# Performance work log

Hardware: AMD Instinct MI355X
Metric: run time of the kernel (lower is better)

## Reference

```python
import jax, jax.numpy as jnp
import numpy as np

BZ, C, H, W, M = 8, 64, 64, 64, 2048  # N = H*W = 4096 scene-graph nodes


def setup_inputs() -> dict:
    key = jax.random.key(0)
    k1, k2 = jax.random.split(key)
    sg_node_feats = jax.random.normal(k1, (BZ, C, H, W), dtype=jnp.float32)
    # weighted adjacency from SG nodes (N) to KG nodes (M)
    sg_kg_adj = jax.random.uniform(k2, (BZ, H * W, M), dtype=jnp.float32)
    return {"sg_node_feats": sg_node_feats, "sg_kg_adj": sg_kg_adj}


def reference(sg_node_feats, sg_kg_adj):
    bz, channels, height, width = sg_node_feats.shape
    x = sg_node_feats.reshape(bz, channels, height * width)  # (bz, C, N)
    degrees = sg_kg_adj.sum(axis=1)                          # (bz, M)
    norm = jnp.maximum(degrees, 1.0)                         # (bz, M)
    # broadcast-multiply + sum over N == batched GEMM (bz,C,N) x (bz,N,M)
    out = jnp.einsum('bcn,bnm->bcm', x, sg_kg_adj) / norm[:, None, :]
    return out.transpose(0, 2, 1)                            # (bz, M, C)
```

## Files before the change

kernel.cpp:

```cpp
#include <hip/hip_runtime.h>


typedef short bf16x8 __attribute__((ext_vector_type(8)));
typedef float f32x4 __attribute__((ext_vector_type(4)));

#define BZc 8
#define Cc 64
#define Nc 4096
#define Mc 2048
#define BMc 64
#define BKc 64
#define KITERS (Nc / BKc)
#define SDW 36

__device__ __forceinline__ unsigned int pkbf(float a, float b) {
  unsigned int ua = __float_as_uint(a) + 0x8000u;
  unsigned int ub = __float_as_uint(b) + 0x8000u;
  return (ua >> 16) | (ub & 0xffff0000u);
}

__global__ __launch_bounds__(512) void sgkg_kernel(
    const float* __restrict__ x,
    const float* __restrict__ adj,
    float* __restrict__ out)
{
  __shared__ unsigned int adjT[BMc * SDW];
  __shared__ float degs[BMc];

  const int t = threadIdx.x;
  const int l = t & 63;
  const int w = t >> 6;

  const int bz     = blockIdx.x >> 5;
  const int m_base = (blockIdx.x & 31) * BMc;

  const int mg  = ((w & 1) << 3) | (l & 7);
  const int p   = ((w >> 1) << 3) | (l >> 3);
  const int sm0 = mg << 2;

  const float* aptr =
      adj + (size_t)bz * Nc * Mc + (size_t)(2 * p) * Mc + (m_base + sm0);
  const int wb = SDW * sm0 + ((((p >> 2) ^ (mg & 7))) << 2) + (p & 3);

  const int m_off = (w & 1) << 5;
  const int c_b   = (w >> 1) << 4;
  const int l15   = l & 15;
  const int l4    = l >> 4;

  const float* xb =
      x + ((size_t)bz * Cc + (c_b + l15)) * Nc + (l4 << 3);

  int aaddr[2][2];
#pragma unroll
  for (int tm = 0; tm < 2; ++tm) {
    const int m  = m_off + tm * 16 + l15;
    const int pi = (m >> 2) & 7;
    aaddr[tm][0] = SDW * m + (((l4) ^ pi) << 2);
    aaddr[tm][1] = SDW * m + (((4 + l4) ^ pi) << 2);
  }

  if (t < BMc) degs[t] = 0.0f;

  f32x4 acc0 = {0.f, 0.f, 0.f, 0.f};
  f32x4 acc1 = {0.f, 0.f, 0.f, 0.f};
  float dacc0 = 0.f, dacc1 = 0.f, dacc2 = 0.f, dacc3 = 0.f;

  float4 r0 = *(const float4*)aptr;
  float4 r1 = *(const float4*)(aptr + Mc);

  for (int it = 0; it < KITERS; ++it) {
    __syncthreads();

    adjT[wb          ] = pkbf(r0.x, r1.x);
    adjT[wb +     SDW] = pkbf(r0.y, r1.y);
    adjT[wb + 2 * SDW] = pkbf(r0.z, r1.z);
    adjT[wb + 3 * SDW] = pkbf(r0.w, r1.w);

    dacc0 += r0.x + r1.x;
    dacc1 += r0.y + r1.y;
    dacc2 += r0.z + r1.z;
    dacc3 += r0.w + r1.w;

    const float* anext = (it + 1 < KITERS) ? (aptr + (size_t)BKc * Mc) : aptr;
    float4 s0 = *(const float4*)anext;
    float4 s1 = *(const float4*)(anext + Mc);

    const float* xit = xb + it * BKc;
    float4 blo0 = *(const float4*)(xit);
    float4 bhi0 = *(const float4*)(xit + 4);
    float4 blo1 = *(const float4*)(xit + 32);
    float4 bhi1 = *(const float4*)(xit + 36);
    union { uint4 u; bf16x8 v; } B0, B1;
    B0.u = make_uint4(pkbf(blo0.x, blo0.y), pkbf(blo0.z, blo0.w),
                      pkbf(bhi0.x, bhi0.y), pkbf(bhi0.z, bhi0.w));
    B1.u = make_uint4(pkbf(blo1.x, blo1.y), pkbf(blo1.z, blo1.w),
                      pkbf(bhi1.x, bhi1.y), pkbf(bhi1.z, bhi1.w));

    __syncthreads();

    bf16x8 a00 = *(const bf16x8*)(adjT + aaddr[0][0]);
    bf16x8 a10 = *(const bf16x8*)(adjT + aaddr[1][0]);
    acc0 = __builtin_amdgcn_mfma_f32_16x16x32_bf16(a00, B0.v, acc0, 0, 0, 0);
    acc1 = __builtin_amdgcn_mfma_f32_16x16x32_bf16(a10, B0.v, acc1, 0, 0, 0);
    bf16x8 a01 = *(const bf16x8*)(adjT + aaddr[0][1]);
    bf16x8 a11 = *(const bf16x8*)(adjT + aaddr[1][1]);
    acc0 = __builtin_amdgcn_mfma_f32_16x16x32_bf16(a01, B1.v, acc0, 0, 0, 0);
    acc1 = __builtin_amdgcn_mfma_f32_16x16x32_bf16(a11, B1.v, acc1, 0, 0, 0);

    aptr = anext;
    r0 = s0;
    r1 = s1;
  }

  __syncthreads();
  atomicAdd(&degs[sm0 + 0], dacc0);
  atomicAdd(&degs[sm0 + 1], dacc1);
  atomicAdd(&degs[sm0 + 2], dacc2);
  atomicAdd(&degs[sm0 + 3], dacc3);
  __syncthreads();

#pragma unroll
  for (int tm = 0; tm < 2; ++tm) {
    const f32x4 acc = tm ? acc1 : acc0;
#pragma unroll
    for (int r = 0; r < 4; ++r) {
      const int ml    = m_off + tm * 16 + (l4 << 2) + r;
      const float nrm = fmaxf(degs[ml], 1.0f);
      const float v   = acc[r] / nrm;
      const size_t o  = ((size_t)(bz * Mc + m_base + ml)) * Cc + (c_b + l15);
      out[o] = v;
    }
  }
}

extern "C" void kernel_launch(void* const* d_in, const int* in_sizes, int n_in,
                              void* d_out, int out_size, void* d_ws, size_t ws_size,
                              hipStream_t stream) {
  const float* x   = (const float*)d_in[0];
  const float* adj = (const float*)d_in[1];
  float* out       = (float*)d_out;
  (void)in_sizes; (void)n_in; (void)out_size; (void)d_ws; (void)ws_size;

  sgkg_kernel<<<dim3(BZc * (Mc / BMc)), dim3(512), 0, stream>>>(x, adj, out);
}
```

Baseline: 378.1 us.

## Split N across blocks, pre-convert x to bf16, double-buffer LDS, add reduce kernel

Adds a pre-pass kernel that converts x to bf16 in workspace so the main loop loads packed bf16 directly instead of converting fp32 every iteration. The main GEMM now uses a split-K over N (two halves) with smaller 32-row M tiles and 256-thread blocks, giving four times as many blocks. The LDS tile is double-buffered, which removes one barrier per iteration. Partial sums and degrees go to workspace and a final kernel adds them and normalizes, at the cost of two extra launches and extra global traffic for the partials.

```diff
diff --git a/kernel.cpp b/kernel.cpp
--- a/kernel.cpp
+++ b/kernel.cpp
@@ -8,10 +8,19 @@
 #define Cc 64
 #define Nc 4096
 #define Mc 2048
-#define BMc 64
+#define BMc 32
 #define BKc 64
-#define KITERS (Nc / BKc)
+#define NSPLIT 2
+#define NSc (Nc / NSPLIT)
+#define KITERS (NSc / BKc)
 #define SDW 36
+#define TILE_DW (BMc * SDW)
+
+#define WS_X_BYTES   (BZc * Cc * Nc * 2)
+#define WS_P_FLOATS  (BZc * Mc * Cc)
+#define WS_P_OFF     (WS_X_BYTES / 4)
+#define WS_D_OFF     (WS_P_OFF + NSPLIT * WS_P_FLOATS)
+#define WS_D_FLOATS  (BZc * Mc)
 
 __device__ __forceinline__ unsigned int pkbf(float a, float b) {
   unsigned int ua = __float_as_uint(a) + 0x8000u;
@@ -19,43 +28,56 @@
   return (ua >> 16) | (ub & 0xffff0000u);
 }
 
-__global__ __launch_bounds__(512) void sgkg_kernel(
-    const float* __restrict__ x,
+__global__ __launch_bounds__(256) void xcvt_kernel(const float* __restrict__ x,
+                                                   unsigned int* __restrict__ xb) {
+  const int i = (blockIdx.x * 256 + threadIdx.x) * 8;
+  float4 a = *(const float4*)(x + i);
+  float4 b = *(const float4*)(x + i + 4);
+  uint4 o = make_uint4(pkbf(a.x, a.y), pkbf(a.z, a.w),
+                       pkbf(b.x, b.y), pkbf(b.z, b.w));
+  *(uint4*)(xb + (i >> 1)) = o;
+}
+
+__global__ __launch_bounds__(256) void sgkg_main(
+    const unsigned int* __restrict__ xbw,
     const float* __restrict__ adj,
-    float* __restrict__ out)
+    float* __restrict__ P,
+    float* __restrict__ D)
 {
-  __shared__ unsigned int adjT[BMc * SDW];
+  __shared__ unsigned int adjT[2][TILE_DW];
   __shared__ float degs[BMc];
 
   const int t = threadIdx.x;
   const int l = t & 63;
   const int w = t >> 6;
 
-  const int bz     = blockIdx.x >> 5;
-  const int m_base = (blockIdx.x & 31) * BMc;
+  const int bz     = blockIdx.x >> 7;
+  const int mb     = (blockIdx.x >> 1) & 63;
+  const int ns     = blockIdx.x & 1;
+  const int m_base = mb * BMc;
+  const int n_base = ns * NSc;
 
-  const int mg  = ((w & 1) << 3) | (l & 7);
-  const int p   = ((w >> 1) << 3) | (l >> 3);
+  const int mg  = l & 7;
+  const int p   = (w << 3) | (l >> 3);
   const int sm0 = mg << 2;
 
   const float* aptr =
-      adj + (size_t)bz * Nc * Mc + (size_t)(2 * p) * Mc + (m_base + sm0);
-  const int wb = SDW * sm0 + ((((p >> 2) ^ (mg & 7))) << 2) + (p & 3);
+      adj + (size_t)bz * Nc * Mc + (size_t)(n_base + 2 * p) * Mc + (m_base + sm0);
+  const int wb = SDW * sm0 + (((p >> 2) ^ mg) << 2) + (p & 3);
 
-  const int m_off = (w & 1) << 5;
-  const int c_b   = (w >> 1) << 4;
-  const int l15   = l & 15;
-  const int l4    = l >> 4;
+  const int c_b = w << 4;
+  const int l15 = l & 15;
+  const int l4  = l >> 4;
 
-  const float* xb =
-      x + ((size_t)bz * Cc + (c_b + l15)) * Nc + (l4 << 3);
+  const uint4* xq = (const uint4*)xbw +
+      (size_t)(bz * Cc + c_b + l15) * (Nc / 8) + (n_base >> 3) + l4;
 
   int aaddr[2][2];
 #pragma unroll
   for (int tm = 0; tm < 2; ++tm) {
-    const int m  = m_off + tm * 16 + l15;
+    const int m  = tm * 16 + l15;
     const int pi = (m >> 2) & 7;
-    aaddr[tm][0] = SDW * m + (((l4) ^ pi) << 2);
+    aaddr[tm][0] = SDW * m + ((l4 ^ pi) << 2);
     aaddr[tm][1] = SDW * m + (((4 + l4) ^ pi) << 2);
   }
 
@@ -69,12 +91,12 @@
   float4 r1 = *(const float4*)(aptr + Mc);
 
   for (int it = 0; it < KITERS; ++it) {
-    __syncthreads();
+    unsigned int* buf = adjT[it & 1];
 
-    adjT[wb          ] = pkbf(r0.x, r1.x);
-    adjT[wb +     SDW] = pkbf(r0.y, r1.y);
-    adjT[wb + 2 * SDW] = pkbf(r0.z, r1.z);
-    adjT[wb + 3 * SDW] = pkbf(r0.w, r1.w);
+    buf[wb          ] = pkbf(r0.x, r1.x);
+    buf[wb +     SDW] = pkbf(r0.y, r1.y);
+    buf[wb + 2 * SDW] = pkbf(r0.z, r1.z);
+    buf[wb + 3 * SDW] = pkbf(r0.w, r1.w);
 
     dacc0 += r0.x + r1.x;
     dacc1 += r0.y + r1.y;
@@ -85,25 +107,19 @@
     float4 s0 = *(const float4*)anext;
     float4 s1 = *(const float4*)(anext + Mc);
 
-    const float* xit = xb + it * BKc;
-    float4 blo0 = *(const float4*)(xit);
-    float4 bhi0 = *(const float4*)(xit + 4);
-    float4 blo1 = *(const float4*)(xit + 32);
-    float4 bhi1 = *(const float4*)(xit + 36);
     union { uint4 u; bf16x8 v; } B0, B1;
-    B0.u = make_uint4(pkbf(blo0.x, blo0.y), pkbf(blo0.z, blo0.w),
-                      pkbf(bhi0.x, bhi0.y), pkbf(bhi0.z, bhi0.w));
-    B1.u = make_uint4(pkbf(blo1.x, blo1.y), pkbf(blo1.z, blo1.w),
-                      pkbf(bhi1.x, bhi1.y), pkbf(bhi1.z, bhi1.w));
+    B0.u = xq[it * 8];
+    B1.u = xq[it * 8 + 4];
 
     __syncthreads();
 
-    bf16x8 a00 = *(const bf16x8*)(adjT + aaddr[0][0]);
-    bf16x8 a10 = *(const bf16x8*)(adjT + aaddr[1][0]);
+    const unsigned int* bufc = buf;
+    bf16x8 a00 = *(const bf16x8*)(bufc + aaddr[0][0]);
+    bf16x8 a10 = *(const bf16x8*)(bufc + aaddr[1][0]);
     acc0 = __builtin_amdgcn_mfma_f32_16x16x32_bf16(a00, B0.v, acc0, 0, 0, 0);
     acc1 = __builtin_amdgcn_mfma_f32_16x16x32_bf16(a10, B0.v, acc1, 0, 0, 0);
-    bf16x8 a01 = *(const bf16x8*)(adjT + aaddr[0][1]);
-    bf16x8 a11 = *(const bf16x8*)(adjT + aaddr[1][1]);
+    bf16x8 a01 = *(const bf16x8*)(bufc + aaddr[0][1]);
+    bf16x8 a11 = *(const bf16x8*)(bufc + aaddr[1][1]);
     acc0 = __builtin_amdgcn_mfma_f32_16x16x32_bf16(a01, B1.v, acc0, 0, 0, 0);
     acc1 = __builtin_amdgcn_mfma_f32_16x16x32_bf16(a11, B1.v, acc1, 0, 0, 0);
 
@@ -118,19 +134,38 @@
   atomicAdd(&degs[sm0 + 2], dacc2);
   atomicAdd(&degs[sm0 + 3], dacc3);
   __syncthreads();
+  if (t < BMc)
+    D[(size_t)ns * WS_D_FLOATS + bz * Mc + m_base + t] = degs[t];
 
 #pragma unroll
   for (int tm = 0; tm < 2; ++tm) {
     const f32x4 acc = tm ? acc1 : acc0;
 #pragma unroll
     for (int r = 0; r < 4; ++r) {
-      const int ml    = m_off + tm * 16 + (l4 << 2) + r;
-      const float nrm = fmaxf(degs[ml], 1.0f);
-      const float v   = acc[r] / nrm;
-      const size_t o  = ((size_t)(bz * Mc + m_base + ml)) * Cc + (c_b + l15);
-      out[o] = v;
+      const int ml   = tm * 16 + (l4 << 2) + r;
+      const size_t o = (size_t)ns * WS_P_FLOATS +
+                       ((size_t)(bz * Mc + m_base + ml)) * Cc + (c_b + l15);
+      P[o] = acc[r];
     }
   }
+}
+
+__global__ __launch_bounds__(256) void fin_kernel(const float* __restrict__ P,
+                                                  const float* __restrict__ D,
+                                                  float* __restrict__ out) {
+  const int g = blockIdx.x * 256 + threadIdx.x;
+  const int e = g * 4;
+  const int bm = e >> 6;
+  const float d   = D[bm] + D[WS_D_FLOATS + bm];
+  const float inv = 1.0f / fmaxf(d, 1.0f);
+  float4 p0 = *(const float4*)(P + e);
+  float4 p1 = *(const float4*)(P + WS_P_FLOATS + e);
+  float4 o;
+  o.x = (p0.x + p1.x) * inv;
+  o.y = (p0.y + p1.y) * inv;
+  o.z = (p0.z + p1.z) * inv;
+  o.w = (p0.w + p1.w) * inv;
+  *(float4*)(out + e) = o;
 }
 
 extern "C" void kernel_launch(void* const* d_in, const int* in_sizes, int n_in,
@@ -139,7 +174,14 @@
   const float* x   = (const float*)d_in[0];
   const float* adj = (const float*)d_in[1];
   float* out       = (float*)d_out;
-  (void)in_sizes; (void)n_in; (void)out_size; (void)d_ws; (void)ws_size;
+  (void)in_sizes; (void)n_in; (void)out_size; (void)ws_size;
 
-  sgkg_kernel<<<dim3(BZc * (Mc / BMc)), dim3(512), 0, stream>>>(x, adj, out);
+  unsigned int* wsX = (unsigned int*)d_ws;
+  float*        wsF = (float*)d_ws;
+  float*        P   = wsF + WS_P_OFF;
+  float*        D   = wsF + WS_D_OFF;
+
+  xcvt_kernel<<<dim3(1024), dim3(256), 0, stream>>>(x, wsX);
+  sgkg_main<<<dim3(BZc * (Mc / BMc) * NSPLIT), dim3(256), 0, stream>>>(wsX, adj, P, D);
+  fin_kernel<<<dim3(1024), dim3(256), 0, stream>>>(P, D, out);
 }
```

Result: slower. 389.2 us (+3.0%).

## Pre-convert x to bf16 and restructure GEMM into barrier-free per-wave tiles

Applied to the files above, without the earlier changes.

A separate pre-pass kernel converts x to packed bf16 in workspace, so the main kernel loads ready-made MFMA operands. The main kernel now gives each wave its own 16-column M tile covering all 64 channels, with a private double-buffered LDS region. This removes every __syncthreads, and degrees are reduced with wave shuffles instead of shared atomics. Adjacency loads are prefetched two iterations ahead to hide latency. The costs are an extra launch, a global round trip for x, and only 256 blocks of 256 threads, which may not fill the machine.

```diff
diff --git a/kernel.cpp b/kernel.cpp
--- a/kernel.cpp
+++ b/kernel.cpp
@@ -8,10 +8,10 @@
 #define Cc 64
 #define Nc 4096
 #define Mc 2048
-#define BMc 64
 #define BKc 64
-#define KITERS (Nc / BKc)
+#define KIT (Nc / BKc)
 #define SDW 36
+#define WTILE (16 * SDW)
 
 __device__ __forceinline__ unsigned int pkbf(float a, float b) {
   unsigned int ua = __float_as_uint(a) + 0x8000u;
@@ -19,116 +19,118 @@
   return (ua >> 16) | (ub & 0xffff0000u);
 }
 
-__global__ __launch_bounds__(512) void sgkg_kernel(
-    const float* __restrict__ x,
+__global__ __launch_bounds__(256) void xcvt_kernel(const float* __restrict__ x,
+                                                   unsigned int* __restrict__ xb) {
+  const int i = (blockIdx.x * 256 + threadIdx.x) * 8;
+  float4 a = *(const float4*)(x + i);
+  float4 b = *(const float4*)(x + i + 4);
+  *(uint4*)(xb + (i >> 1)) = make_uint4(pkbf(a.x, a.y), pkbf(a.z, a.w),
+                                        pkbf(b.x, b.y), pkbf(b.z, b.w));
+}
+
+__global__ __launch_bounds__(256) void sgkg_main(
+    const uint4* __restrict__ X,
     const float* __restrict__ adj,
     float* __restrict__ out)
 {
-  __shared__ unsigned int adjT[BMc * SDW];
-  __shared__ float degs[BMc];
+  __shared__ unsigned int adjT[4][2][WTILE];
 
   const int t = threadIdx.x;
   const int l = t & 63;
   const int w = t >> 6;
 
-  const int bz     = blockIdx.x >> 5;
-  const int m_base = (blockIdx.x & 31) * BMc;
+  const int W      = blockIdx.x * 4 + w;
+  const int bz     = W >> 7;
+  const int m_base = (W & 127) << 4;
 
-  const int mg  = ((w & 1) << 3) | (l & 7);
-  const int p   = ((w >> 1) << 3) | (l >> 3);
-  const int sm0 = mg << 2;
+  const int mg  = l & 3;
+  const int pp  = l >> 2;
+  const int l15 = l & 15;
+  const int l4  = l >> 4;
 
-  const float* aptr =
-      adj + (size_t)bz * Nc * Mc + (size_t)(2 * p) * Mc + (m_base + sm0);
-  const int wb = SDW * sm0 + ((((p >> 2) ^ (mg & 7))) << 2) + (p & 3);
+  const float* ap = adj + (size_t)bz * Nc * Mc + (size_t)(4 * pp) * Mc
+                        + (m_base + (mg << 2));
+  const size_t tstep = (size_t)BKc * Mc;
 
-  const int m_off = (w & 1) << 5;
-  const int c_b   = (w >> 1) << 4;
-  const int l15   = l & 15;
-  const int l4    = l >> 4;
+  unsigned int* wbuf0 = &adjT[w][0][0];
+  unsigned int* wbuf1 = &adjT[w][1][0];
+  const int wb = SDW * (mg << 2) + (((pp >> 1) ^ mg) << 2) + ((pp & 1) << 1);
 
-  const float* xb =
-      x + ((size_t)bz * Cc + (c_b + l15)) * Nc + (l4 << 3);
+  const int pi  = l15 >> 2;
+  const int ra0 = SDW * l15 + ((l4 ^ pi) << 2);
+  const int ra1 = SDW * l15 + (((4 + l4) ^ pi) << 2);
 
-  int aaddr[2][2];
+  const uint4* xq0 = X + (size_t)(bz * Cc +  0 + l15) * (Nc / 8) + l4;
+  const uint4* xq1 = X + (size_t)(bz * Cc + 16 + l15) * (Nc / 8) + l4;
+  const uint4* xq2 = X + (size_t)(bz * Cc + 32 + l15) * (Nc / 8) + l4;
+  const uint4* xq3 = X + (size_t)(bz * Cc + 48 + l15) * (Nc / 8) + l4;
+
+  f32x4 acc0 = {0.f,0.f,0.f,0.f}, acc1 = {0.f,0.f,0.f,0.f};
+  f32x4 acc2 = {0.f,0.f,0.f,0.f}, acc3 = {0.f,0.f,0.f,0.f};
+  float d0 = 0.f, d1 = 0.f, d2 = 0.f, d3 = 0.f;
+
+  float4 A0[4], A1[4];
 #pragma unroll
-  for (int tm = 0; tm < 2; ++tm) {
-    const int m  = m_off + tm * 16 + l15;
-    const int pi = (m >> 2) & 7;
-    aaddr[tm][0] = SDW * m + (((l4) ^ pi) << 2);
-    aaddr[tm][1] = SDW * m + (((4 + l4) ^ pi) << 2);
+  for (int q = 0; q < 4; ++q) A0[q] = *(const float4*)(ap + q * Mc);
+#pragma unroll
+  for (int q = 0; q < 4; ++q) A1[q] = *(const float4*)(ap + tstep + q * Mc);
+
+#define HALF(IT, AR, BUF)                                                      \
+  {                                                                            \
+    const int bix = (IT) << 3;                                                 \
+    uint4 Bv0 = xq0[bix],     Bv1 = xq1[bix],     Bv2 = xq2[bix],     Bv3 = xq3[bix];     \
+    uint4 Bv4 = xq0[bix + 4], Bv5 = xq1[bix + 4], Bv6 = xq2[bix + 4], Bv7 = xq3[bix + 4]; \
+    *(uint2*)(BUF + wb          ) = make_uint2(pkbf(AR[0].x, AR[1].x), pkbf(AR[2].x, AR[3].x)); \
+    *(uint2*)(BUF + wb + SDW    ) = make_uint2(pkbf(AR[0].y, AR[1].y), pkbf(AR[2].y, AR[3].y)); \
+    *(uint2*)(BUF + wb + 2 * SDW) = make_uint2(pkbf(AR[0].z, AR[1].z), pkbf(AR[2].z, AR[3].z)); \
+    *(uint2*)(BUF + wb + 3 * SDW) = make_uint2(pkbf(AR[0].w, AR[1].w), pkbf(AR[2].w, AR[3].w)); \
+    d0 += AR[0].x + AR[1].x + AR[2].x + AR[3].x;                               \
+    d1 += AR[0].y + AR[1].y + AR[2].y + AR[3].y;                               \
+    d2 += AR[0].z + AR[1].z + AR[2].z + AR[3].z;                               \
+    d3 += AR[0].w + AR[1].w + AR[2].w + AR[3].w;                               \
+    {                                                                          \
+      const int nt = ((IT) + 2 < KIT) ? (IT) + 2 : KIT - 1;                    \
+      const float* pf = ap + (size_t)nt * tstep;                               \
+      _Pragma("unroll")                                                        \
+      for (int q = 0; q < 4; ++q) AR[q] = *(const float4*)(pf + q * Mc);       \
+    }                                                                          \
+    union { uint4 u; bf16x8 v; } bb;                                           \
+    bf16x8 af0 = *(const bf16x8*)(BUF + ra0);                                  \
+    bb.u = Bv0; acc0 = __builtin_amdgcn_mfma_f32_16x16x32_bf16(af0, bb.v, acc0, 0, 0, 0); \
+    bb.u = Bv1; acc1 = __builtin_amdgcn_mfma_f32_16x16x32_bf16(af0, bb.v, acc1, 0, 0, 0); \
+    bb.u = Bv2; acc2 = __builtin_amdgcn_mfma_f32_16x16x32_bf16(af0, bb.v, acc2, 0, 0, 0); \
+    bb.u = Bv3; acc3 = __builtin_amdgcn_mfma_f32_16x16x32_bf16(af0, bb.v, acc3, 0, 0, 0); \
+    bf16x8 af1 = *(const bf16x8*)(BUF + ra1);                                  \
+    bb.u = Bv4; acc0 = __builtin_amdgcn_mfma_f32_16x16x32_bf16(af1, bb.v, acc0, 0, 0, 0); \
+    bb.u = Bv5; acc1 = __builtin_amdgcn_mfma_f32_16x16x32_bf16(af1, bb.v, acc1, 0, 0, 0); \
+    bb.u = Bv6; acc2 = __builtin_amdgcn_mfma_f32_16x16x32_bf16(af1, bb.v, acc2, 0, 0, 0); \
+    bb.u = Bv7; acc3 = __builtin_amdgcn_mfma_f32_16x16x32_bf16(af1, bb.v, acc3, 0, 0, 0); \
   }
 
-  if (t < BMc) degs[t] = 0.0f;
+  for (int it = 0; it < KIT; it += 2) {
+    HALF(it,     A0, wbuf0)
+    HALF(it + 1, A1, wbuf1)
+  }
+#undef HALF
 
-  f32x4 acc0 = {0.f, 0.f, 0.f, 0.f};
-  f32x4 acc1 = {0.f, 0.f, 0.f, 0.f};
-  float dacc0 = 0.f, dacc1 = 0.f, dacc2 = 0.f, dacc3 = 0.f;
+  d0 += __shfl_xor(d0, 4);  d0 += __shfl_xor(d0, 8);  d0 += __shfl_xor(d0, 16); d0 += __shfl_xor(d0, 32);
+  d1 += __shfl_xor(d1, 4);  d1 += __shfl_xor(d1, 8);  d1 += __shfl_xor(d1, 16); d1 += __shfl_xor(d1, 32);
+  d2 += __shfl_xor(d2, 4);  d2 += __shfl_xor(d2, 8);  d2 += __shfl_xor(d2, 16); d2 += __shfl_xor(d2, 32);
+  d3 += __shfl_xor(d3, 4);  d3 += __shfl_xor(d3, 8);  d3 += __shfl_xor(d3, 16); d3 += __shfl_xor(d3, 32);
 
-  float4 r0 = *(const float4*)aptr;
-  float4 r1 = *(const float4*)(aptr + Mc);
+  float inv0 = 1.0f / fmaxf(__shfl(d0, l4), 1.0f);
+  float inv1 = 1.0f / fmaxf(__shfl(d1, l4), 1.0f);
+  float inv2 = 1.0f / fmaxf(__shfl(d2, l4), 1.0f);
+  float inv3 = 1.0f / fmaxf(__shfl(d3, l4), 1.0f);
 
-  for (int it = 0; it < KITERS; ++it) {
-    __syncthreads();
-
-    adjT[wb          ] = pkbf(r0.x, r1.x);
-    adjT[wb +     SDW] = pkbf(r0.y, r1.y);
-    adjT[wb + 2 * SDW] = pkbf(r0.z, r1.z);
-    adjT[wb + 3 * SDW] = pkbf(r0.w, r1.w);
-
-    dacc0 += r0.x + r1.x;
-    dacc1 += r0.y + r1.y;
-    dacc2 += r0.z + r1.z;
-    dacc3 += r0.w + r1.w;
-
-    const float* anext = (it + 1 < KITERS) ? (aptr + (size_t)BKc * Mc) : aptr;
-    float4 s0 = *(const float4*)anext;
-    float4 s1 = *(const float4*)(anext + Mc);
-
-    const float* xit = xb + it * BKc;
-    float4 blo0 = *(const float4*)(xit);
-    float4 bhi0 = *(const float4*)(xit + 4);
-    float4 blo1 = *(const float4*)(xit + 32);
-    float4 bhi1 = *(const float4*)(xit + 36);
-    union { uint4 u; bf16x8 v; } B0, B1;
-    B0.u = make_uint4(pkbf(blo0.x, blo0.y), pkbf(blo0.z, blo0.w),
-                      pkbf(bhi0.x, bhi0.y), pkbf(bhi0.z, bhi0.w));
-    B1.u = make_uint4(pkbf(blo1.x, blo1.y), pkbf(blo1.z, blo1.w),
-                      pkbf(bhi1.x, bhi1.y), pkbf(bhi1.z, bhi1.w));
-
-    __syncthreads();
-
-    bf16x8 a00 = *(const bf16x8*)(adjT + aaddr[0][0]);
-    bf16x8 a10 = *(const bf16x8*)(adjT + aaddr[1][0]);
-    acc0 = __builtin_amdgcn_mfma_f32_16x16x32_bf16(a00, B0.v, acc0, 0, 0, 0);
-    acc1 = __builtin_amdgcn_mfma_f32_16x16x32_bf16(a10, B0.v, acc1, 0, 0, 0);
-    bf16x8 a01 = *(const bf16x8*)(adjT + aaddr[0][1]);
-    bf16x8 a11 = *(const bf16x8*)(adjT + aaddr[1][1]);
-    acc0 = __builtin_amdgcn_mfma_f32_16x16x32_bf16(a01, B1.v, acc0, 0, 0, 0);
-    acc1 = __builtin_amdgcn_mfma_f32_16x16x32_bf16(a11, B1.v, acc1, 0, 0, 0);
-
-    aptr = anext;
-    r0 = s0;
-    r1 = s1;
-  }
-
-  __syncthreads();
-  atomicAdd(&degs[sm0 + 0], dacc0);
-  atomicAdd(&degs[sm0 + 1], dacc1);
-  atomicAdd(&degs[sm0 + 2], dacc2);
-  atomicAdd(&degs[sm0 + 3], dacc3);
-  __syncthreads();
-
+  const size_t ob = (size_t)(bz * Mc + m_base + (l4 << 2)) * Cc + l15;
+  f32x4 av[4] = {acc0, acc1, acc2, acc3};
+  float iv[4] = {inv0, inv1, inv2, inv3};
 #pragma unroll
-  for (int tm = 0; tm < 2; ++tm) {
-    const f32x4 acc = tm ? acc1 : acc0;
+  for (int ct = 0; ct < 4; ++ct) {
 #pragma unroll
     for (int r = 0; r < 4; ++r) {
-      const int ml    = m_off + tm * 16 + (l4 << 2) + r;
-      const float nrm = fmaxf(degs[ml], 1.0f);
-      const float v   = acc[r] / nrm;
-      const size_t o  = ((size_t)(bz * Mc + m_base + ml)) * Cc + (c_b + l15);
-      out[o] = v;
+      out[ob + (size_t)r * Cc + (ct << 4)] = av[ct][r] * iv[r];
     }
   }
 }
@@ -139,7 +141,10 @@
   const float* x   = (const float*)d_in[0];
   const float* adj = (const float*)d_in[1];
   float* out       = (float*)d_out;
-  (void)in_sizes; (void)n_in; (void)out_size; (void)d_ws; (void)ws_size;
+  (void)in_sizes; (void)n_in; (void)out_size; (void)ws_size;
 
-  sgkg_kernel<<<dim3(BZc * (Mc / BMc)), dim3(512), 0, stream>>>(x, adj, out);
+  unsigned int* wsX = (unsigned int*)d_ws;
+
+  xcvt_kernel<<<dim3(1024), dim3(256), 0, stream>>>(x, wsX);
+  sgkg_main<<<dim3(256), dim3(256), 0, stream>>>((const uint4*)wsX, adj, out);
 }
```

Result: slower. 409.8 us (+8.4%).
